# Optimization experiments

Hardware: AMD Instinct MI355X
Metric: run time of the kernel (lower is better)

The kernel has to match this reference:

```python
import jax, jax.numpy as jnp
import numpy as np

SHAPES = ((8, 24, 24), (4, 12, 12), (2, 6, 6), (1, 3, 3))  # (D, H, W) per level
D_MODEL = 256
N_HEADS = 8
HEAD_DIM = D_MODEL // N_HEADS
N_LEVELS = 4
N_POINTS = 4
N_LAYERS = 6
D_FFN = 1024


def setup_inputs():
    key = jax.random.key(0)
    ks = iter(jax.random.split(key, 64))
    def rn(shape, s=1.0):
        return jax.random.normal(next(ks), shape, jnp.float32) * s
    inp = {}
    for i, (D, H, W) in enumerate(SHAPES):
        inp[f'src{i}'] = rn((2, 4, D_MODEL, D, H, W))
        inp[f'pos{i}'] = rn((2, 4, D_MODEL, D, H, W), 0.1)
    HLP3 = N_HEADS * N_LEVELS * N_POINTS * 3
    HLP = N_HEADS * N_LEVELS * N_POINTS
    L = N_LAYERS
    inp['level_embed'] = rn((N_LEVELS, D_MODEL), 0.02)
    inp['W_off'] = rn((L, D_MODEL, HLP3), 0.01)
    inp['b_off'] = rn((L, HLP3), 0.5)
    inp['W_attn'] = rn((L, D_MODEL, HLP), 0.02)
    inp['b_attn'] = jnp.zeros((L, HLP), jnp.float32)
    inp['W_val'] = rn((L, D_MODEL, D_MODEL), 0.02)
    inp['b_val'] = jnp.zeros((L, D_MODEL), jnp.float32)
    inp['W_out'] = rn((L, D_MODEL, D_MODEL), 0.02)
    inp['b_out'] = jnp.zeros((L, D_MODEL), jnp.float32)
    inp['g1'] = jnp.ones((L, D_MODEL), jnp.float32)
    inp['be1'] = jnp.zeros((L, D_MODEL), jnp.float32)
    inp['W1'] = rn((L, D_MODEL, D_FFN), 0.02)
    inp['b1'] = jnp.zeros((L, D_FFN), jnp.float32)
    inp['W2'] = rn((L, D_FFN, D_MODEL), 0.02)
    inp['b2'] = jnp.zeros((L, D_MODEL), jnp.float32)
    inp['g2'] = jnp.ones((L, D_MODEL), jnp.float32)
    inp['be2'] = jnp.zeros((L, D_MODEL), jnp.float32)
    return inp


def _layer_norm(x, g, b):
    m = jnp.mean(x, -1, keepdims=True)
    v = jnp.mean((x - m) ** 2, -1, keepdims=True)
    return (x - m) * jax.lax.rsqrt(v + 1e-5) * g + b


def _sample_level(v, loc, aw, D, H, W):
    # v: (B, nH, D*H*W, hd)   loc: (B, Lq, nH, P, 3) in [0,1] as (x,y,z)
    # aw: (B, Lq, nH, P) attention weights for this level
    # Trilinear sampling matching grid_sample(align_corners=False, padding_mode='zeros').
    B, Lq, nH, P, _ = loc.shape
    hd = v.shape[-1]
    x = loc[..., 0] * W - 0.5
    y = loc[..., 1] * H - 0.5
    z = loc[..., 2] * D - 0.5
    x0, y0, z0 = jnp.floor(x), jnp.floor(y), jnp.floor(z)
    fx, fy, fz = x - x0, y - y0, z - z0
    awt = aw.transpose(0, 2, 1, 3)  # (B, nH, Lq, P)
    out = jnp.zeros((B, nH, Lq, hd), v.dtype)
    for dz in (0, 1):
        for dy in (0, 1):
            for dx in (0, 1):
                xi, yi, zi = x0 + dx, y0 + dy, z0 + dz
                w = (fx if dx else 1.0 - fx) * (fy if dy else 1.0 - fy) * (fz if dz else 1.0 - fz)
                valid = (xi >= 0) & (xi < W) & (yi >= 0) & (yi < H) & (zi >= 0) & (zi < D)
                w = (w * valid).transpose(0, 2, 1, 3) * awt  # fold attn weight in
                idx = ((jnp.clip(zi, 0, D - 1) * H + jnp.clip(yi, 0, H - 1)) * W
                       + jnp.clip(xi, 0, W - 1)).astype(jnp.int32)
                idx = idx.transpose(0, 2, 1, 3).reshape(B, nH, Lq * P)
                g = jnp.take_along_axis(v, idx[..., None], 2).reshape(B, nH, Lq, P, hd)
                out = out + jnp.einsum('bhqpc,bhqp->bhqc', g, w)
    return out


def _msda(q, x, ref, Woff, boff, Wat, bat, Wv, bv, Wo, bo):
    B, Lq, _ = q.shape
    value = (x @ Wv + bv).reshape(B, Lq, N_HEADS, HEAD_DIM)
    off = (q @ Woff + boff).reshape(B, Lq, N_HEADS, N_LEVELS, N_POINTS, 3)
    attn = jax.nn.softmax((q @ Wat + bat).reshape(B, Lq, N_HEADS, N_LEVELS * N_POINTS), -1)
    attn = attn.reshape(B, Lq, N_HEADS, N_LEVELS, N_POINTS)
    # offset normalizer in (x, y, z) = (W, H, D) order per level
    norm = jnp.array([[W, H, D] for (D, H, W) in SHAPES], dtype=q.dtype)
    loc = ref[:, :, None, :, None, :] + off / norm[None, None, None, :, None, :]
    out = jnp.zeros((B, N_HEADS, Lq, HEAD_DIM), q.dtype)
    start = 0
    for lv, (D, H, W) in enumerate(SHAPES):
        n = D * H * W
        v_l = value[:, start:start + n].transpose(0, 2, 1, 3)  # (B, nH, n, hd)
        fn = jax.checkpoint(lambda v_, l_, a_, D=D, H=H, W=W: _sample_level(v_, l_, a_, D, H, W))
        out = out + fn(v_l, loc[:, :, :, lv], attn[:, :, :, lv])
        start += n
    return out.transpose(0, 2, 1, 3).reshape(B, Lq, D_MODEL) @ Wo + bo


def _forward(src0, src1, src2, src3, pos0, pos1, pos2, pos3, level_embed,
             W_off, b_off, W_attn, b_attn, W_val, b_val, W_out, b_out,
             g1, be1, W1, b1, W2, b2, g2, be2):
    srcs = [src0, src1, src2, src3]
    poss = [pos0, pos1, pos2, pos3]
    bs, nf = src0.shape[0], src0.shape[1]
    xs, ps = [], []
    for lvl in range(N_LEVELS):
        s, p = srcs[lvl], poss[lvl]
        b, n, c = s.shape[:3]
        xs.append(s.reshape(b, n, c, -1).transpose(0, 1, 3, 2))
        ps.append(p.reshape(b, n, c, -1).transpose(0, 1, 3, 2) + level_embed[lvl])
    x = jnp.concatenate(xs, 2)    # (bs, nf, Len, C)
    pos = jnp.concatenate(ps, 2)
    Len = x.shape[2]
    B = bs * nf
    x = x.reshape(B, Len, D_MODEL)
    pos = pos.reshape(B, Len, D_MODEL)
    # reference points; masks are all-False so valid_ratios == 1
    refs = []
    for (D, H, W) in SHAPES:
        rz, ry, rx = jnp.meshgrid(
            (jnp.arange(D, dtype=jnp.float32) + 0.5) / D,
            (jnp.arange(H, dtype=jnp.float32) + 0.5) / H,
            (jnp.arange(W, dtype=jnp.float32) + 0.5) / W,
            indexing='ij')
        refs.append(jnp.stack([rx.ravel(), ry.ravel(), rz.ravel()], -1))
    ref = jnp.concatenate(refs, 0)  # (Len, 3)
    ref = jnp.broadcast_to(ref[None, :, None, :], (B, Len, N_LEVELS, 3))
    for l in range(N_LAYERS):
        q = x + pos
        a = _msda(q, x, ref, W_off[l], b_off[l], W_attn[l], b_attn[l],
                  W_val[l], b_val[l], W_out[l], b_out[l])
        x = _layer_norm(x + a, g1[l], be1[l])
        ff = jax.nn.relu(x @ W1[l] + b1[l]) @ W2[l] + b2[l]
        x = _layer_norm(x + ff, g2[l], be2[l])
    return x.reshape(bs, nf, Len, D_MODEL)


def reference(src0, src1, src2, src3, pos0, pos1, pos2, pos3, level_embed,
              W_off, b_off, W_attn, b_attn, W_val, b_val, W_out, b_out,
              g1, be1, W1, b1, W2, b2, g2, be2):
    return _forward(src0, src1, src2, src3, pos0, pos1, pos2, pos3, level_embed,
                    W_off, b_off, W_attn, b_attn, W_val, b_val, W_out, b_out,
                    g1, be1, W1, b1, W2, b2, g2, be2)
```

## Files before the change

kernel.cpp:

```cpp
#include <hip/hip_runtime.h>
#include <hip/hip_fp16.h>

constexpr int LEN = 5265;
constexpr long NTOK = 8L * LEN;

typedef float f32x4 __attribute__((ext_vector_type(4)));
typedef unsigned int u32x4 __attribute__((ext_vector_type(4)));

static __device__ __forceinline__ unsigned short f2bf(float f) {
    unsigned u = __float_as_uint(f);
    unsigned r = (u + 0x7FFFu + ((u >> 16) & 1u)) >> 16;
    return (unsigned short)r;
}
static __device__ __forceinline__ float uasf(unsigned u) { return __uint_as_float(u); }

#if __has_builtin(__builtin_amdgcn_global_load_lds)
#define HAS_GLL 1
static __device__ __forceinline__ void gll16(const void* g, void* l) {
    __builtin_amdgcn_global_load_lds(
        (const __attribute__((address_space(1))) void*)g,
        (__attribute__((address_space(3))) void*)l, 16, 0, 0);
}
#else
#define HAS_GLL 0
#endif

__global__ __launch_bounds__(256) void pack_kernel(
    const float* __restrict__ s0, const float* __restrict__ s1,
    const float* __restrict__ s2, const float* __restrict__ s3,
    const float* __restrict__ p0, const float* __restrict__ p1,
    const float* __restrict__ p2, const float* __restrict__ p3,
    const float* __restrict__ lev,
    float* __restrict__ x, float* __restrict__ pos,
    unsigned short* __restrict__ xbf, unsigned short* __restrict__ qbf)
{
    long t = (long)blockIdx.x * 256 + threadIdx.x;
    if (t >= NTOK * 256) return;
    int c = (int)(t & 255);
    long r = t >> 8;
    int q = (int)(r % LEN);
    int B = (int)(r / LEN);
    int lvl, base, n;
    const float *sp, *pp;
    if (q < 4608)      { lvl = 0; base = 0;    n = 4608; sp = s0; pp = p0; }
    else if (q < 5184) { lvl = 1; base = 4608; n = 576;  sp = s1; pp = p1; }
    else if (q < 5256) { lvl = 2; base = 5184; n = 72;   sp = s2; pp = p2; }
    else               { lvl = 3; base = 5256; n = 9;    sp = s3; pp = p3; }
    int s = q - base;
    long si = ((long)B * 256 + c) * n + s;
    float xv = sp[si];
    float pv = pp[si] + lev[lvl * 256 + c];
    x[t] = xv;
    pos[t] = pv;
    xbf[t] = f2bf(xv);
    qbf[t] = f2bf(xv + pv);
}

__global__ __launch_bounds__(64) void ref_kernel(float* __restrict__ refb)
{
    int q = blockIdx.x * 64 + threadIdx.x;
    if (q >= LEN) return;
    int base, D_, H_, W_;
    if (q < 4608)      { base = 0;    D_ = 8; H_ = 24; W_ = 24; }
    else if (q < 5184) { base = 4608; D_ = 4; H_ = 12; W_ = 12; }
    else if (q < 5256) { base = 5184; D_ = 2; H_ = 6;  W_ = 6;  }
    else               { base = 5256; D_ = 1; H_ = 3;  W_ = 3;  }
    int s = q - base;
    int hw = H_ * W_;
    int z = s / hw; int rem = s - z * hw;
    int y = rem / W_; int xx = rem - y * W_;
    refb[q * 3 + 0] = (xx + 0.5f) / (float)W_;
    refb[q * 3 + 1] = (y + 0.5f) / (float)H_;
    refb[q * 3 + 2] = (z + 0.5f) / (float)D_;
}

__global__ __launch_bounds__(256) void wtrans_kernel(
    const float* __restrict__ src, unsigned short* __restrict__ dst,
    int K, int N, long dstLS)
{
    __shared__ float t[32][33];
    const int k0 = blockIdx.x * 32, n0 = blockIdx.y * 32;
    src += (long)blockIdx.z * K * N;
    dst += (long)blockIdx.z * dstLS;
    const int tx = threadIdx.x, ty = threadIdx.y;
    for (int i = ty; i < 32; i += 8)
        t[i][tx] = src[(long)(k0 + i) * N + n0 + tx];
    __syncthreads();
    for (int i = ty; i < 32; i += 8)
        dst[(long)(n0 + i) * K + k0 + tx] = f2bf(t[tx][i]);
}

static __device__ __forceinline__ int swz(int m) { return (m ^ (m >> 2)) & 3; }

template<bool OUTBF, bool RELU>
__global__ __launch_bounds__(256) void mfma_gemm(
    const unsigned short* __restrict__ A, const unsigned short* __restrict__ Wt,
    const float* __restrict__ bias, const float* __restrict__ bias2, int nb0,
    void* __restrict__ Cv, int M, int K, int N)
{
    __shared__ u32x4 a_l[512];
    __shared__ u32x4 b_l[512];
    const int tid = threadIdx.x;
    const int row0 = blockIdx.x * 128;
    const int col0 = blockIdx.y * 128;
    const int wave = tid >> 6, lane = tid & 63;
    const int wr = wave >> 1, wc = wave & 1;
    const int l15 = lane & 15, l4 = lane >> 4;

    f32x4 acc[4][4];
#pragma unroll
    for (int i = 0; i < 4; ++i)
#pragma unroll
        for (int j = 0; j < 4; ++j) acc[i][j] = (f32x4){0.f, 0.f, 0.f, 0.f};

    const int sm0 = tid >> 2, sk = tid & 3;
    const int swk = (sk ^ swz(sm0)) * 8;
    const int arA0 = min(row0 + sm0, M - 1);
    const int arA1 = min(row0 + sm0 + 64, M - 1);
    const unsigned short* gA0 = A  + (long)arA0 * K + swk;
    const unsigned short* gA1 = A  + (long)arA1 * K + swk;
    const unsigned short* gB0 = Wt + (long)(col0 + sm0) * K + swk;
    const unsigned short* gB1 = Wt + (long)(col0 + sm0 + 64) * K + swk;

    for (int k0 = 0; k0 < K; k0 += 32) {
        __syncthreads();
#if HAS_GLL
        gll16(gA0 + k0, &a_l[wave * 64]);
        gll16(gA1 + k0, &a_l[256 + wave * 64]);
        gll16(gB0 + k0, &b_l[wave * 64]);
        gll16(gB1 + k0, &b_l[256 + wave * 64]);
#else
        a_l[tid]       = *(const u32x4*)(gA0 + k0);
        a_l[256 + tid] = *(const u32x4*)(gA1 + k0);
        b_l[tid]       = *(const u32x4*)(gB0 + k0);
        b_l[256 + tid] = *(const u32x4*)(gB1 + k0);
#endif
        __syncthreads();
        u32x4 af[4], bfr[4];
#pragma unroll
        for (int i = 0; i < 4; ++i) {
            const int m = wr * 64 + i * 16 + l15;
            af[i] = a_l[m * 4 + (l4 ^ swz(m))];
            const int n = wc * 64 + i * 16 + l15;
            bfr[i] = b_l[n * 4 + (l4 ^ swz(n))];
        }
#pragma unroll
        for (int i = 0; i < 4; ++i)
#pragma unroll
            for (int j = 0; j < 4; ++j)
                asm volatile("v_mfma_f32_16x16x32_bf16 %0, %1, %2, %0"
                             : "+v"(acc[i][j]) : "v"(af[i]), "v"(bfr[j]));
    }

    float* Cf = (float*)Cv;
    unsigned short* Cb = (unsigned short*)Cv;
    const int cb = col0 + wc * 64;
    float bj[4];
#pragma unroll
    for (int j = 0; j < 4; ++j) {
        const int col = cb + j * 16 + l15;
        bj[j] = (col < nb0) ? bias[col] : bias2[col - nb0];
    }
#pragma unroll
    for (int i = 0; i < 4; ++i) {
        const int rb = row0 + wr * 64 + i * 16 + l4 * 4;
#pragma unroll
        for (int r = 0; r < 4; ++r) {
            const int row = rb + r;
            if (row < M) {
#pragma unroll
                for (int j = 0; j < 4; ++j) {
                    const int col = cb + j * 16 + l15;
                    float v = acc[i][j][r] + bj[j];
                    if (RELU) v = fmaxf(v, 0.f);
                    if (OUTBF) Cb[(long)row * N + col] = f2bf(v);
                    else       Cf[(long)row * N + col] = v;
                }
            }
        }
    }
}

__global__ __launch_bounds__(256) void msda_sample_kernel(
    const unsigned short* __restrict__ value,
    const float* __restrict__ obuf,
    const float* __restrict__ refb,
    unsigned short* __restrict__ outb)
{
    __shared__ unsigned s_wi[32][8][17];
    const int tid = threadIdx.x;
    const long gid0 = (long)blockIdx.x * 32;

#pragma unroll
    for (int jj = 0; jj < 2; ++jj) {
        const int j = tid + jj * 256;
        const int g = j >> 4, pt = j & 15;
        const long gg = gid0 + g;
        const int h = (int)(gg & 7);
        const long tok = gg >> 3;
        const int q = (int)(tok % LEN);
        const int b = (int)(tok / LEN);

        const float* lg = &obuf[tok * 512 + 384 + h * 16];
        float mx = lg[0];
#pragma unroll
        for (int k = 1; k < 16; ++k) mx = fmaxf(mx, lg[k]);
        float den = 0.f;
#pragma unroll
        for (int k = 0; k < 16; ++k) den += __expf(lg[k] - mx);
        const float aw = __expf(lg[pt] - mx) / den;

        const int lvl = pt >> 2;
        int D_, H_, W_, base;
        if (lvl == 0)      { D_ = 8; H_ = 24; W_ = 24; base = 0; }
        else if (lvl == 1) { D_ = 4; H_ = 12; W_ = 12; base = 4608; }
        else if (lvl == 2) { D_ = 2; H_ = 6;  W_ = 6;  base = 5184; }
        else               { D_ = 1; H_ = 3;  W_ = 3;  base = 5256; }
        const float fW = (float)W_, fH = (float)H_, fD = (float)D_;

        const float* op = &obuf[tok * 512 + h * 48 + pt * 3];
        const float X = (refb[q * 3 + 0] + op[0] / fW) * fW - 0.5f;
        const float Y = (refb[q * 3 + 1] + op[1] / fH) * fH - 0.5f;
        const float Z = (refb[q * 3 + 2] + op[2] / fD) * fD - 0.5f;
        const float x0f = floorf(X), y0f = floorf(Y), z0f = floorf(Z);
        const float fx = X - x0f, fy = Y - y0f, fz = Z - z0f;
        const int x0 = (int)x0f, y0 = (int)y0f, z0 = (int)z0f;
#pragma unroll
        for (int c = 0; c < 8; ++c) {
            const int dx = c & 1, dy = (c >> 1) & 1, dz = c >> 2;
            const int xi = x0 + dx, yi = y0 + dy, zi = z0 + dz;
            float w = (dx ? fx : 1.f - fx) * (dy ? fy : 1.f - fy) * (dz ? fz : 1.f - fz);
            const bool valid = (xi >= 0) && (xi < W_) && (yi >= 0) && (yi < H_) &&
                               (zi >= 0) && (zi < D_);
            const int xc = min(max(xi, 0), W_ - 1);
            const int yc = min(max(yi, 0), H_ - 1);
            const int zc = min(max(zi, 0), D_ - 1);
            const int n = (zc * H_ + yc) * W_ + xc;
            const unsigned short ti = (unsigned short)(b * LEN + base + n);
            const unsigned short hw =
                __half_as_ushort(__float2half_rn(valid ? w * aw : 0.f));
            s_wi[g][c][pt] = ((unsigned)ti << 16) | (unsigned)hw;
        }
    }
    __syncthreads();

    const int g = tid >> 3, d4 = tid & 7;
    const long gg = gid0 + g;
    const int h = (int)(gg & 7);
    const char* vbase = (const char*)value + h * 64 + d4 * 8;
    const unsigned* sp = &s_wi[g][0][0];
    float a0 = 0.f, a1 = 0.f, a2 = 0.f, a3 = 0.f;
#pragma unroll
    for (int c = 0; c < 8; ++c) {
#pragma unroll
        for (int pt = 0; pt < 16; ++pt) {
            const unsigned word = sp[c * 17 + pt];
            const float w = __half2float(__ushort_as_half((unsigned short)word));
            const uint2 v = *(const uint2*)(vbase + ((word >> 16) << 9));
            a0 += w * uasf(v.x << 16);
            a1 += w * uasf(v.x & 0xffff0000u);
            a2 += w * uasf(v.y << 16);
            a3 += w * uasf(v.y & 0xffff0000u);
        }
    }
    ushort4 o;
    o.x = f2bf(a0); o.y = f2bf(a1); o.z = f2bf(a2); o.w = f2bf(a3);
    *(ushort4*)&outb[gg * 32 + d4 * 4] = o;
}

template<bool NEEDQ>
__global__ __launch_bounds__(256) void resid_ln_kernel(
    float* __restrict__ x, const float* __restrict__ r, const float* __restrict__ pos,
    const float* __restrict__ g, const float* __restrict__ be,
    unsigned short* __restrict__ xbf, unsigned short* __restrict__ qbf)
{
    const long tok = (long)blockIdx.x * 4 + (threadIdx.x >> 6);
    const int lane = threadIdx.x & 63;
    if (tok >= NTOK) return;
    const float4 xv = *(const float4*)&x[tok * 256 + lane * 4];
    const float4 rv = *(const float4*)&r[tok * 256 + lane * 4];
    float s0 = xv.x + rv.x, s1 = xv.y + rv.y, s2 = xv.z + rv.z, s3 = xv.w + rv.w;
    float sum = s0 + s1 + s2 + s3;
#pragma unroll
    for (int o = 32; o > 0; o >>= 1) sum += __shfl_xor(sum, o);
    const float mean = sum * (1.f / 256.f);
    const float d0 = s0 - mean, d1 = s1 - mean, d2 = s2 - mean, d3 = s3 - mean;
    float vs = d0 * d0 + d1 * d1 + d2 * d2 + d3 * d3;
#pragma unroll
    for (int o = 32; o > 0; o >>= 1) vs += __shfl_xor(vs, o);
    const float rstd = rsqrtf(vs * (1.f / 256.f) + 1e-5f);
    float4 o4;
    o4.x = d0 * rstd * g[lane * 4 + 0] + be[lane * 4 + 0];
    o4.y = d1 * rstd * g[lane * 4 + 1] + be[lane * 4 + 1];
    o4.z = d2 * rstd * g[lane * 4 + 2] + be[lane * 4 + 2];
    o4.w = d3 * rstd * g[lane * 4 + 3] + be[lane * 4 + 3];
    *(float4*)&x[tok * 256 + lane * 4] = o4;
    ushort4 xb;
    xb.x = f2bf(o4.x); xb.y = f2bf(o4.y); xb.z = f2bf(o4.z); xb.w = f2bf(o4.w);
    *(ushort4*)&xbf[tok * 256 + lane * 4] = xb;
    if (NEEDQ) {
        const float4 pv = *(const float4*)&pos[tok * 256 + lane * 4];
        ushort4 qb;
        qb.x = f2bf(o4.x + pv.x); qb.y = f2bf(o4.y + pv.y);
        qb.z = f2bf(o4.z + pv.z); qb.w = f2bf(o4.w + pv.w);
        *(ushort4*)&qbf[tok * 256 + lane * 4] = qb;
    }
}

extern "C" void kernel_launch(void* const* d_in, const int* in_sizes, int n_in,
                              void* d_out, int out_size, void* d_ws, size_t ws_size,
                              hipStream_t stream)
{
    (void)n_in; (void)out_size; (void)ws_size;
    const float* src[4];
    const float* posin[4];
    const bool interleaved = (in_sizes[1] == in_sizes[0]);
    for (int i = 0; i < 4; ++i) {
        if (interleaved) { src[i] = (const float*)d_in[2 * i]; posin[i] = (const float*)d_in[2 * i + 1]; }
        else             { src[i] = (const float*)d_in[i];     posin[i] = (const float*)d_in[4 + i]; }
    }
    const float* lev    = (const float*)d_in[8];
    const float* W_off  = (const float*)d_in[9];
    const float* b_off  = (const float*)d_in[10];
    const float* W_attn = (const float*)d_in[11];
    const float* b_attn = (const float*)d_in[12];
    const float* W_val  = (const float*)d_in[13];
    const float* b_val  = (const float*)d_in[14];
    const float* W_out  = (const float*)d_in[15];
    const float* b_out  = (const float*)d_in[16];
    const float* g1     = (const float*)d_in[17];
    const float* be1    = (const float*)d_in[18];
    const float* W1     = (const float*)d_in[19];
    const float* b1     = (const float*)d_in[20];
    const float* W2     = (const float*)d_in[21];
    const float* b2     = (const float*)d_in[22];
    const float* g2     = (const float*)d_in[23];
    const float* be2    = (const float*)d_in[24];

    float* xbuf = (float*)d_out;
    char* p = (char*)d_ws;
    float* posb = (float*)p;            p += NTOK * 256 * 4;
    float* tmp  = (float*)p;
    unsigned short* valueb = (unsigned short*)tmp;
                                        p += NTOK * 256 * 4;
    float* obuf = (float*)p;
    unsigned short* hidden = (unsigned short*)obuf;
                                        p += NTOK * 512 * 4;
    unsigned short* msdabf = (unsigned short*)p;  p += NTOK * 256 * 2;
    unsigned short* xbf    = (unsigned short*)p;  p += NTOK * 256 * 2;
    unsigned short* qbf    = (unsigned short*)p;  p += NTOK * 256 * 2;
    unsigned short* wt_val = (unsigned short*)p;  p += 6L * 256 * 256 * 2;
    unsigned short* wt_oa  = (unsigned short*)p;  p += 6L * 512 * 256 * 2;
    unsigned short* wt_out = (unsigned short*)p;  p += 6L * 256 * 256 * 2;
    unsigned short* wt_w1  = (unsigned short*)p;  p += 6L * 1024 * 256 * 2;
    unsigned short* wt_w2  = (unsigned short*)p;  p += 6L * 256 * 1024 * 2;
    float* refb = (float*)p;            p += LEN * 3 * 4;

    pack_kernel<<<(int)((NTOK * 256) / 256), 256, 0, stream>>>(
        src[0], src[1], src[2], src[3], posin[0], posin[1], posin[2], posin[3],
        lev, xbuf, posb, xbf, qbf);
    ref_kernel<<<(LEN + 63) / 64, 64, 0, stream>>>(refb);
    dim3 tb(32, 8);
    wtrans_kernel<<<dim3(8, 8, 6),  tb, 0, stream>>>(W_val,  wt_val, 256, 256,  65536);
    wtrans_kernel<<<dim3(8, 12, 6), tb, 0, stream>>>(W_off,  wt_oa,  256, 384,  131072);
    wtrans_kernel<<<dim3(8, 4, 6),  tb, 0, stream>>>(W_attn, wt_oa + 384 * 256, 256, 128, 131072);
    wtrans_kernel<<<dim3(8, 8, 6),  tb, 0, stream>>>(W_out,  wt_out, 256, 256,  65536);
    wtrans_kernel<<<dim3(8, 32, 6), tb, 0, stream>>>(W1,     wt_w1,  256, 1024, 262144);
    wtrans_kernel<<<dim3(32, 8, 6), tb, 0, stream>>>(W2,     wt_w2,  1024, 256, 262144);

    const int MT = (int)((NTOK + 127) / 128);
    const int BIG = 1 << 30;
    for (int l = 0; l < 6; ++l) {
        mfma_gemm<true, false><<<dim3(MT, 2), 256, 0, stream>>>(
            xbf, wt_val + (long)l * 65536, b_val + l * 256, b_val + l * 256, BIG,
            valueb, (int)NTOK, 256, 256);
        mfma_gemm<false, false><<<dim3(MT, 4), 256, 0, stream>>>(
            qbf, wt_oa + (long)l * 131072, b_off + l * 384, b_attn + l * 128, 384,
            obuf, (int)NTOK, 256, 512);
        msda_sample_kernel<<<(int)(NTOK / 4), 256, 0, stream>>>(
            valueb, obuf, refb, msdabf);
        mfma_gemm<false, false><<<dim3(MT, 2), 256, 0, stream>>>(
            msdabf, wt_out + (long)l * 65536, b_out + l * 256, b_out + l * 256, BIG,
            tmp, (int)NTOK, 256, 256);
        resid_ln_kernel<false><<<(int)((NTOK + 3) / 4), 256, 0, stream>>>(
            xbuf, tmp, posb, g1 + l * 256, be1 + l * 256, xbf, qbf);
        mfma_gemm<true, true><<<dim3(MT, 8), 256, 0, stream>>>(
            xbf, wt_w1 + (long)l * 262144, b1 + l * 1024, b1 + l * 1024, BIG,
            hidden, (int)NTOK, 256, 1024);
        mfma_gemm<false, false><<<dim3(MT, 2), 256, 0, stream>>>(
            hidden, wt_w2 + (long)l * 262144, b2 + l * 256, b2 + l * 256, BIG,
            tmp, (int)NTOK, 1024, 256);
        resid_ln_kernel<true><<<(int)((NTOK + 3) / 4), 256, 0, stream>>>(
            xbuf, tmp, posb, g2 + l * 256, be2 + l * 256, xbf, qbf);
    }
}
```

Baseline: 2.593 ms.

## Store value projection in fp32 and restructure MSDA sampling per thread

The value GEMM now writes fp32 instead of bf16, and the sampling kernel reads two float4 vectors per sample, each thread covering 8 channels over 64 head-groups per block. The per-point softmax over 16 logits now uses shuffle reductions instead of each thread re-reading all 16. The aim is to cut redundant logit loads and bf16 unpacking and to widen the gathers. In exchange, the value tensor doubles in size, so gather traffic rises, and the token index is still packed into 16 bits of the shared-memory word.

```diff
diff --git a/kernel.cpp b/kernel.cpp
--- a/kernel.cpp
+++ b/kernel.cpp
@@ -12,7 +12,6 @@
     unsigned r = (u + 0x7FFFu + ((u >> 16) & 1u)) >> 16;
     return (unsigned short)r;
 }
-static __device__ __forceinline__ float uasf(unsigned u) { return __uint_as_float(u); }
 
 #if __has_builtin(__builtin_amdgcn_global_load_lds)
 #define HAS_GLL 1
@@ -182,18 +181,18 @@
 }
 
 __global__ __launch_bounds__(256) void msda_sample_kernel(
-    const unsigned short* __restrict__ value,
+    const float* __restrict__ value,
     const float* __restrict__ obuf,
     const float* __restrict__ refb,
     unsigned short* __restrict__ outb)
 {
-    __shared__ unsigned s_wi[32][8][17];
+    __shared__ unsigned s_wi[64 * 137];
     const int tid = threadIdx.x;
-    const long gid0 = (long)blockIdx.x * 32;
-
-#pragma unroll
-    for (int jj = 0; jj < 2; ++jj) {
-        const int j = tid + jj * 256;
+    const long gid0 = (long)blockIdx.x * 64;
+
+#pragma unroll
+    for (int jj = 0; jj < 4; ++jj) {
+        const int j = jj * 256 + tid;
         const int g = j >> 4, pt = j & 15;
         const long gg = gid0 + g;
         const int h = (int)(gg & 7);
@@ -201,14 +200,15 @@
         const int q = (int)(tok % LEN);
         const int b = (int)(tok / LEN);
 
-        const float* lg = &obuf[tok * 512 + 384 + h * 16];
-        float mx = lg[0];
-#pragma unroll
-        for (int k = 1; k < 16; ++k) mx = fmaxf(mx, lg[k]);
-        float den = 0.f;
-#pragma unroll
-        for (int k = 0; k < 16; ++k) den += __expf(lg[k] - mx);
-        const float aw = __expf(lg[pt] - mx) / den;
+        const float lgv = obuf[tok * 512 + 384 + h * 16 + pt];
+        float m = lgv;
+#pragma unroll
+        for (int o = 1; o < 16; o <<= 1) m = fmaxf(m, __shfl_xor(m, o));
+        const float e = __expf(lgv - m);
+        float den = e;
+#pragma unroll
+        for (int o = 1; o < 16; o <<= 1) den += __shfl_xor(den, o);
+        const float aw = e / den;
 
         const int lvl = pt >> 2;
         int D_, H_, W_, base;
@@ -236,36 +236,39 @@
             const int yc = min(max(yi, 0), H_ - 1);
             const int zc = min(max(zi, 0), D_ - 1);
             const int n = (zc * H_ + yc) * W_ + xc;
-            const unsigned short ti = (unsigned short)(b * LEN + base + n);
+            const unsigned ti = (unsigned)(b * LEN + base + n);
             const unsigned short hw =
                 __half_as_ushort(__float2half_rn(valid ? w * aw : 0.f));
-            s_wi[g][c][pt] = ((unsigned)ti << 16) | (unsigned)hw;
+            s_wi[g * 137 + c * 17 + pt] = (ti << 16) | (unsigned)hw;
         }
     }
     __syncthreads();
 
-    const int g = tid >> 3, d4 = tid & 7;
+    const int g = tid >> 2, d8 = tid & 3;
     const long gg = gid0 + g;
     const int h = (int)(gg & 7);
-    const char* vbase = (const char*)value + h * 64 + d4 * 8;
-    const unsigned* sp = &s_wi[g][0][0];
-    float a0 = 0.f, a1 = 0.f, a2 = 0.f, a3 = 0.f;
-#pragma unroll
-    for (int c = 0; c < 8; ++c) {
-#pragma unroll
-        for (int pt = 0; pt < 16; ++pt) {
-            const unsigned word = sp[c * 17 + pt];
-            const float w = __half2float(__ushort_as_half((unsigned short)word));
-            const uint2 v = *(const uint2*)(vbase + ((word >> 16) << 9));
-            a0 += w * uasf(v.x << 16);
-            a1 += w * uasf(v.x & 0xffff0000u);
-            a2 += w * uasf(v.y << 16);
-            a3 += w * uasf(v.y & 0xffff0000u);
-        }
-    }
-    ushort4 o;
-    o.x = f2bf(a0); o.y = f2bf(a1); o.z = f2bf(a2); o.w = f2bf(a3);
-    *(ushort4*)&outb[gg * 32 + d4 * 4] = o;
+    const float* vbase = value + h * 32 + d8 * 8;
+    const unsigned* sp = &s_wi[g * 137];
+    float a[8];
+#pragma unroll
+    for (int k = 0; k < 8; ++k) a[k] = 0.f;
+#pragma unroll 16
+    for (int i = 0; i < 128; ++i) {
+        const unsigned word = sp[i + (i >> 4)];
+        const float w = __half2float(__ushort_as_half((unsigned short)word));
+        const float* vp = vbase + ((long)(word >> 16) << 8);
+        const f32x4 v0 = *(const f32x4*)vp;
+        const f32x4 v1 = *(const f32x4*)(vp + 4);
+#pragma unroll
+        for (int k = 0; k < 4; ++k) a[k] += w * v0[k];
+#pragma unroll
+        for (int k = 0; k < 4; ++k) a[4 + k] += w * v1[k];
+    }
+    u32x4 o;
+#pragma unroll
+    for (int k = 0; k < 4; ++k)
+        o[k] = (unsigned)f2bf(a[2 * k]) | ((unsigned)f2bf(a[2 * k + 1]) << 16);
+    *(u32x4*)&outb[gg * 32 + d8 * 8] = o;
 }
 
 template<bool NEEDQ>
@@ -341,7 +344,7 @@
     char* p = (char*)d_ws;
     float* posb = (float*)p;            p += NTOK * 256 * 4;
     float* tmp  = (float*)p;
-    unsigned short* valueb = (unsigned short*)tmp;
+    float* valuef = tmp;
                                         p += NTOK * 256 * 4;
     float* obuf = (float*)p;
     unsigned short* hidden = (unsigned short*)obuf;
@@ -371,14 +374,14 @@
     const int MT = (int)((NTOK + 127) / 128);
     const int BIG = 1 << 30;
     for (int l = 0; l < 6; ++l) {
-        mfma_gemm<true, false><<<dim3(MT, 2), 256, 0, stream>>>(
+        mfma_gemm<false, false><<<dim3(MT, 2), 256, 0, stream>>>(
             xbf, wt_val + (long)l * 65536, b_val + l * 256, b_val + l * 256, BIG,
-            valueb, (int)NTOK, 256, 256);
+            valuef, (int)NTOK, 256, 256);
         mfma_gemm<false, false><<<dim3(MT, 4), 256, 0, stream>>>(
             qbf, wt_oa + (long)l * 131072, b_off + l * 384, b_attn + l * 128, 384,
             obuf, (int)NTOK, 256, 512);
-        msda_sample_kernel<<<(int)(NTOK / 4), 256, 0, stream>>>(
-            valueb, obuf, refb, msdabf);
+        msda_sample_kernel<<<(int)(NTOK / 8), 256, 0, stream>>>(
+            valuef, obuf, refb, msdabf);
         mfma_gemm<false, false><<<dim3(MT, 2), 256, 0, stream>>>(
             msdabf, wt_out + (long)l * 65536, b_out + l * 256, b_out + l * 256, BIG,
             tmp, (int)NTOK, 256, 256);
```

New measurement: 2.628 ms. About the same (+1.3%).
